# Optimization experiments

Hardware: AMD Instinct MI355X
Metric: run time of the kernel (lower is better)

## Reference

```python
import jax, jax.numpy as jnp
import numpy as np

L, S, H = 65536, 4, 256
WID = H // 2


def _linear(x, W, b):
    # eqx.nn.Linear: y = W @ x + b, W is (out, in)
    return jnp.einsum('...i,oi->...o', x, W) + b


def setup_inputs() -> dict:
    key = jax.random.key(0)
    ks = jax.random.split(key, 22)
    w = lambda k, shape: (jax.random.normal(k, shape, jnp.float32) * 0.02)
    return {
        'h': jax.random.normal(ks[0], (L, H), jnp.float32),
        'obs_stack': jax.random.normal(ks[1], (L, S, H), jnp.float32),
        'staleness_stack': jax.random.uniform(ks[2], (L, S), jnp.float32, 0.0, 10.0),
        'valid_stack': jax.random.bernoulli(ks[3], 0.8, (L, S)),
        'Wq': w(ks[4], (H, H)), 'bq': jnp.zeros((H,), jnp.float32),
        'Wk': w(ks[5], (H, H)), 'bk': jnp.zeros((H,), jnp.float32),
        'Wv': w(ks[6], (H, H)), 'bv': jnp.zeros((H,), jnp.float32),
        'null_key': jax.random.normal(ks[7], (H,), jnp.float32),
        'null_value': jax.random.normal(ks[8], (H,), jnp.float32),
        'mlp_w0': w(ks[9], (WID, 1)), 'mlp_b0': jnp.zeros((WID,), jnp.float32),
        'mlp_w1': w(ks[10], (WID, WID)), 'mlp_b1': jnp.zeros((WID,), jnp.float32),
        'mlp_w2': w(ks[11], (H, WID)), 'mlp_b2': jnp.zeros((H,), jnp.float32),
        'Wg': w(ks[12], (H, 2 * H)), 'bg': jnp.zeros((H,), jnp.float32),
        'ln_w': jnp.ones((H,), jnp.float32), 'ln_b': jnp.zeros((H,), jnp.float32),
    }


def reference(h, obs_stack, staleness_stack, valid_stack,
              Wq, bq, Wk, bk, Wv, bv, null_key, null_value,
              mlp_w0, mlp_b0, mlp_w1, mlp_b1, mlp_w2, mlp_b2,
              Wg, bg, ln_w, ln_b):
    Hd = h.shape[-1]
    Ln = h.shape[0]
    # staleness MLP (depth=2 hidden layers, relu)
    x = jnp.log1p(staleness_stack)[..., None]            # [L,S,1]
    x = jax.nn.relu(_linear(x, mlp_w0, mlp_b0))          # [L,S,W]
    x = jax.nn.relu(_linear(x, mlp_w1, mlp_b1))          # [L,S,W]
    st_emb = _linear(x, mlp_w2, mlp_b2)                  # [L,S,H]
    mod = obs_stack + st_emb
    q = _linear(h, Wq, bq)                               # [L,H]
    k = _linear(mod, Wk, bk)                             # [L,S,H]
    v = _linear(mod, Wv, bv)                             # [L,S,H]
    k = jnp.concatenate([k, jnp.broadcast_to(null_key, (Ln, 1, Hd))], axis=1)
    v = jnp.concatenate([v, jnp.broadcast_to(null_value, (Ln, 1, Hd))], axis=1)
    vmask = jnp.concatenate([valid_stack, jnp.ones((Ln, 1), bool)], axis=1)
    scores = jnp.einsum('lh,lsh->ls', q, k) / jnp.sqrt(jnp.float32(Hd))
    scores = scores + jnp.where(vmask, 0.0, -5.0)
    weights = jax.nn.softmax(scores, axis=-1)            # [L,S+1]
    fused = jnp.einsum('ls,lsh->lh', weights, v)         # [L,H]
    gate = jax.nn.sigmoid(_linear(jnp.concatenate([h, fused], axis=-1), Wg, bg))
    any_real = jnp.any(vmask[:, :-1], axis=-1, keepdims=True)
    gate = gate * any_real.astype(gate.dtype)
    mu = jnp.mean(fused, axis=-1, keepdims=True)
    var = jnp.mean((fused - mu) ** 2, axis=-1, keepdims=True)
    update = (fused - mu) / jnp.sqrt(var + 1e-5) * ln_w + ln_b
    return h + gate * update
```

## Files before the change

### kernel.cpp

```cpp
#include <hip/hip_runtime.h>
#include <math.h>


typedef __bf16 bf16x8 __attribute__((ext_vector_type(8)));
typedef float f32x4 __attribute__((ext_vector_type(4)));
typedef unsigned short u16;
typedef unsigned short u16x4 __attribute__((ext_vector_type(4)));

constexpr int Tr = 32;

constexpr int OFF_BQK = 16;
constexpr int OFF_NBK = 272;
constexpr int OFF_NQ  = 528;
constexpr int OFF_VB2P = 784;
constexpr int OFF_SCC = 1040;
constexpr size_t UOFF_QK  = 0;
constexpr size_t UOFF_X2W = 65536;
constexpr size_t UOFF_QK2 = 81920;
constexpr size_t UOFF_V   = 114688;
constexpr size_t UOFF_V2  = 180224;
constexpr size_t UOFF_G   = 212992;

constexpr int SH_QK  = 0;
constexpr int SH_QK2 = 8192;
constexpr int SH_OB  = 12288;
constexpr int SMEM_BYTES = 40960 + (384 + 128) * 4;

__device__ __forceinline__ float4 ld4(const float* p) { return *reinterpret_cast<const float4*>(p); }
__device__ __forceinline__ u16 f2bf(float x) { __bf16 b = (__bf16)x; return __builtin_bit_cast(u16, b); }
__device__ __forceinline__ float bf2f(u16 u) {
  unsigned v = ((unsigned)u) << 16;
  return __builtin_bit_cast(float, v);
}
__device__ __forceinline__ f32x4 mfma16(bf16x8 a, bf16x8 b, f32x4 c) {
  return __builtin_amdgcn_mfma_f32_16x16x32_bf16(a, b, c, 0, 0, 0);
}
__device__ __forceinline__ bf16x8 ldA8(const u16* su, int base, int stride, int row, int kcol) {
  int off = (row * stride + kcol) ^ ((row & 7) << 3);
  return *reinterpret_cast<const bf16x8*>(su + base + off);
}
__device__ __forceinline__ bf16x8 ldB8(const u16* p, size_t off) {
  return *reinterpret_cast<const bf16x8*>(p + off);
}
__device__ __forceinline__ void stBF(u16* su, int base, int stride, int row, int col, float v) {
  int off = (row * stride + col) ^ ((row & 7) << 3);
  su[base + off] = f2bf(v);
}
__device__ __forceinline__ bf16x8 ldHfrag(const float* __restrict__ h, size_t row, int k) {
  const float4 a = ld4(h + row * 256 + k);
  const float4 b = ld4(h + row * 256 + k + 4);
  bf16x8 r;
  r[0] = (__bf16)a.x; r[1] = (__bf16)a.y; r[2] = (__bf16)a.z; r[3] = (__bf16)a.w;
  r[4] = (__bf16)b.x; r[5] = (__bf16)b.y; r[6] = (__bf16)b.z; r[7] = (__bf16)b.w;
  return r;
}
__device__ __forceinline__ void barrier_lds() {
  asm volatile("s_waitcnt lgkmcnt(0)" ::: "memory");
  __builtin_amdgcn_s_barrier();
  asm volatile("" ::: "memory");
}

__global__ void k_zero(int* __restrict__ f) {
  if (threadIdx.x == 0) f[0] = 0;
}
__global__ void k_flag(const unsigned int* __restrict__ v, int nwords, int* __restrict__ flag_out) {
  int my = 0;
  for (int i = blockIdx.x * blockDim.x + threadIdx.x; i < nwords; i += gridDim.x * blockDim.x) {
    const unsigned int w = v[i];
    if (w > 1u) my |= 1;
    if (((w & 0xFFu) > 1u) || (((w >> 8) & 0xFFu) > 1u) || (((w >> 16) & 0xFFu) > 1u) ||
        ((w >> 24) > 1u))
      my |= 2;
  }
  my |= __shfl_xor(my, 32, 64);
  my |= __shfl_xor(my, 16, 64);
  my |= __shfl_xor(my, 8, 64);
  my |= __shfl_xor(my, 4, 64);
  my |= __shfl_xor(my, 2, 64);
  my |= __shfl_xor(my, 1, 64);
  if ((threadIdx.x & 63) == 0 && my) atomicOr(flag_out, my);
}

__global__ void k_prep(const float* __restrict__ Wq, const float* __restrict__ bq,
                       const float* __restrict__ Wk, const float* __restrict__ bk,
                       const float* __restrict__ Wv, const float* __restrict__ bv,
                       const float* __restrict__ nk, const float* __restrict__ w1,
                       const float* __restrict__ w2, const float* __restrict__ b2,
                       const float* __restrict__ Wg, float* __restrict__ W) {
  const int b = blockIdx.x, t = threadIdx.x;
  u16* Wu = (u16*)(W + 2048);
  __shared__ float s_tile[48 * 260];
  if (b < 672) {
    int gemm, nt, kt, KT;
    size_t ubase;
    if (b < 128)      { gemm = 0; KT = 8;  kt = b & 7;          nt = b >> 3;          ubase = UOFF_QK; }
    else if (b < 160) { gemm = 1; KT = 4;  kt = (b - 128) & 3;  nt = (b - 128) >> 2;  ubase = UOFF_X2W; }
    else if (b < 224) { gemm = 2; KT = 8;  kt = (b - 160) & 7;  nt = (b - 160) >> 3;  ubase = UOFF_QK2; }
    else if (b < 352) { gemm = 3; KT = 8;  kt = (b - 224) & 7;  nt = (b - 224) >> 3;  ubase = UOFF_V; }
    else if (b < 416) { gemm = 4; KT = 4;  kt = (b - 352) & 3;  nt = (b - 352) >> 2;  ubase = UOFF_V2; }
    else              { gemm = 5; KT = 16; kt = (b - 416) & 15; nt = (b - 416) >> 4;  ubase = UOFF_G; }
    if (gemm == 0 || gemm == 4) {
      float* sA = s_tile;
      float* sB = s_tile + 16 * 260;
      const int n0 = nt * 16, k0 = kt * 32;
      if (gemm == 0) {
        for (int idx = t; idx < 4096; idx += 256) {
          const int o = idx >> 4, n = idx & 15;
          sA[n * 260 + o] = Wk[o * 256 + n0 + n];
        }
        for (int idx = t; idx < 8192; idx += 256) {
          const int o = idx >> 5, k = idx & 31;
          sB[k * 260 + o] = Wq[o * 256 + k0 + k];
        }
      } else {
        for (int idx = t; idx < 4096; idx += 256) {
          const int n = idx >> 8, o = idx & 255;
          sA[n * 260 + o] = Wv[(size_t)(n0 + n) * 256 + o];
        }
        for (int idx = t; idx < 8192; idx += 256) {
          const int o = idx >> 5, k = idx & 31;
          sB[k * 260 + o] = w2[o * 128 + k0 + k];
        }
      }
      __syncthreads();
      for (int e = t; e < 512; e += 256) {
        const int l = e >> 3, j = e & 7;
        const int n = l & 15;
        const int k = ((l >> 4) << 3) + j;
        const float4* pa = (const float4*)(sA + n * 260);
        const float4* pb = (const float4*)(sB + k * 260);
        float acc = 0.f;
#pragma unroll 8
        for (int o4 = 0; o4 < 64; ++o4) {
          const float4 a = pa[o4], bb = pb[o4];
          acc += a.x * bb.x + a.y * bb.y + a.z * bb.z + a.w * bb.w;
        }
        Wu[ubase + (size_t)(nt * KT + kt) * 512 + e] = f2bf(acc);
      }
    } else {
      for (int e = t; e < 512; e += 256) {
        const int l = e >> 3, j = e & 7;
        const int n = nt * 16 + (l & 15);
        const int k = kt * 32 + ((l >> 4) << 3) + j;
        float val;
        if (gemm == 1)      val = w1[n * 128 + k];
        else if (gemm == 2) val = w2[k * 128 + n];
        else if (gemm == 3) val = Wv[n * 256 + k];
        else                val = Wg[n * 512 + k];
        Wu[ubase + (size_t)(nt * KT + kt) * 512 + e] = f2bf(val);
      }
    }
  } else {
    float* s_u = s_tile;
    float a = 0.f;
    for (int hh = 0; hh < 256; ++hh) a = fmaf(Wk[t * 256 + hh], b2[hh], a);
    s_u[t] = a + bk[t];
    __syncthreads();
    float a1 = 0.f, a2 = 0.f, a3 = 0.f, a4 = 0.f;
    for (int o = 0; o < 256; ++o) {
      a1 = fmaf(Wq[o * 256 + t], s_u[o], a1);
      a2 = fmaf(Wq[o * 256 + t], nk[o], a2);
      a3 = fmaf(Wk[o * 256 + t], bq[o], a3);
      a4 = fmaf(Wv[t * 256 + o], b2[o], a4);
    }
    W[OFF_NBK + t] = a1;
    W[OFF_NQ + t] = a2;
    W[OFF_BQK + t] = a3;
    W[OFF_VB2P + t] = a4 + bv[t];
    if (t == 0) {
      float c1 = 0.f, c2 = 0.f;
      for (int o = 0; o < 256; ++o) {
        c1 = fmaf(bq[o], s_u[o], c1);
        c2 = fmaf(bq[o], nk[o], c2);
      }
      W[OFF_SCC] = c1;
      W[OFF_SCC + 1] = c2;
    }
  }
}

__launch_bounds__(512) __global__
void k_main(const float* __restrict__ h, const float* __restrict__ obs,
            const float* __restrict__ stal, const void* __restrict__ valid,
            const float* __restrict__ w0, const float* __restrict__ b0,
            const float* __restrict__ b1, const float* __restrict__ bg,
            const float* __restrict__ lnw, const float* __restrict__ lnb,
            const float* __restrict__ nv, const float* __restrict__ W,
            const int* __restrict__ flagp, float* __restrict__ out) {
  extern __shared__ char smraw[];
  u16* su = (u16*)smraw;
  float* s_sc = (float*)(smraw + 40960);
  float* s_x0 = s_sc + 384;
  const u16* Wu = (const u16*)(W + 2048);
  const int t = threadIdx.x;
  const int lane = t & 63, wv = t >> 6;
  const int l16 = lane & 15, g = lane >> 4;
  const size_t row0 = (size_t)blockIdx.x * Tr;
  const int vv = *flagp;
  const int mode = ((vv & 1) == 0) ? 0 : (((vv & 2) == 0) ? 1 : 2);

  if (t < 128) {
    const int r = t >> 2, s = t & 3;
    const size_t idx = (row0 + r) * 4 + s;
    bool vb;
    if (mode == 0) vb = ((const int*)valid)[idx] != 0;
    else if (mode == 1) vb = ((const unsigned char*)valid)[idx] != 0;
    else vb = ((const float*)valid)[idx] != 0.f;
    s_sc[r * 12 + s] = vb ? 0.f : -5.f;
    s_x0[t] = log1pf(stal[idx]);
  } else if (t < 160) {
    const int r = t - 128;
    const size_t base = (row0 + r) * 4;
    bool any = false;
    for (int s = 0; s < 4; ++s) {
      bool vb;
      if (mode == 0) vb = ((const int*)valid)[base + s] != 0;
      else if (mode == 1) vb = ((const unsigned char*)valid)[base + s] != 0;
      else vb = ((const float*)valid)[base + s] != 0.f;
      any |= vb;
    }
    s_sc[r * 12 + 6] = any ? 1.f : 0.f;
  }
  barrier_lds();

  {
    const int task = lane >> 3, sub = lane & 7;
    const int r = wv * 4 + (task >> 1);
    const int which = task & 1;
    const float* vecp = which ? (W + OFF_NQ) : (W + OFF_NBK);
    const float* hp = h + (row0 + r) * 256 + sub * 32;
    const float* vp = vecp + sub * 32;
    float acc = 0.f;
#pragma unroll
    for (int j = 0; j < 8; ++j) {
      const float4 hv = ld4(hp + j * 4);
      const float4 vvv = ld4(vp + j * 4);
      acc += hv.x * vvv.x + hv.y * vvv.y + hv.z * vvv.z + hv.w * vvv.w;
    }
    acc += __shfl_xor(acc, 1, 64);
    acc += __shfl_xor(acc, 2, 64);
    acc += __shfl_xor(acc, 4, 64);
    if (sub == 0) s_sc[r * 12 + 4 + which] = acc + W[OFF_SCC + which];
  }
  {
    f32x4 acc[2][2] = {{{0.f,0.f,0.f,0.f},{0.f,0.f,0.f,0.f}},
                       {{0.f,0.f,0.f,0.f},{0.f,0.f,0.f,0.f}}};
#pragma unroll
    for (int kt = 0; kt < 8; ++kt) {
      const bf16x8 a0 = ldHfrag(h, row0 + l16, kt * 32 + g * 8);
      const bf16x8 a1 = ldHfrag(h, row0 + 16 + l16, kt * 32 + g * 8);
#pragma unroll
      for (int n2 = 0; n2 < 2; ++n2) {
        const int nt = wv * 2 + n2;
        const bf16x8 b = ldB8(Wu, UOFF_QK + (size_t)((nt * 8 + kt) * 64 + lane) * 8);
        acc[0][n2] = mfma16(a0, b, acc[0][n2]);
        acc[1][n2] = mfma16(a1, b, acc[1][n2]);
      }
    }
#pragma unroll
    for (int n2 = 0; n2 < 2; ++n2) {
      const int col = (wv * 2 + n2) * 16 + l16;
      const float bqk = W[OFF_BQK + col];
#pragma unroll
      for (int mt = 0; mt < 2; ++mt)
#pragma unroll
        for (int reg = 0; reg < 4; ++reg)
          stBF(su, SH_QK, 256, mt * 16 + g * 4 + reg, col, acc[mt][n2][reg] + bqk);
    }
  }
  bf16x8 Bq2[8];
  {
    const int ntp = (wv & 3) * 2;
#pragma unroll
    for (int i = 0; i < 8; ++i) {
      const int kt = i >> 1, n2 = i & 1;
      Bq2[i] = ldB8(Wu, UOFF_QK2 + (size_t)(((ntp + n2) * 8 + kt) * 64 + lane) * 8);
    }
  }
  barrier_lds();

  u16x4 x2p[8];
  float4 ob01[8];
  {
    const int mt = wv >> 2, ntp = (wv & 3) * 2;
    f32x4 acc2[2] = {{0.f, 0.f, 0.f, 0.f}, {0.f, 0.f, 0.f, 0.f}};
#pragma unroll
    for (int kt = 0; kt < 8; ++kt) {
      const bf16x8 a = ldA8(su, SH_QK, 256, mt * 16 + l16, kt * 32 + g * 8);
#pragma unroll
      for (int n2 = 0; n2 < 2; ++n2) {
        bf16x8 b;
        if (kt < 4) b = Bq2[kt * 2 + n2];
        else b = ldB8(Wu, UOFF_QK2 + (size_t)(((ntp + n2) * 8 + kt) * 64 + lane) * 8);
        acc2[n2] = mfma16(a, b, acc2[n2]);
      }
    }
    f32x4 accx[8] = {{0.f,0.f,0.f,0.f},{0.f,0.f,0.f,0.f},{0.f,0.f,0.f,0.f},{0.f,0.f,0.f,0.f},
                     {0.f,0.f,0.f,0.f},{0.f,0.f,0.f,0.f},{0.f,0.f,0.f,0.f},{0.f,0.f,0.f,0.f}};
    const float x0v = s_x0[wv * 16 + l16];
#pragma unroll
    for (int kt = 0; kt < 4; ++kt) {
      const int k0 = kt * 32 + g * 8;
      const float4 wa = ld4(w0 + k0), wb = ld4(w0 + k0 + 4);
      const float4 ba = ld4(b0 + k0), bb = ld4(b0 + k0 + 4);
      bf16x8 a;
      a[0] = (__bf16)fmaxf(fmaf(wa.x, x0v, ba.x), 0.f);
      a[1] = (__bf16)fmaxf(fmaf(wa.y, x0v, ba.y), 0.f);
      a[2] = (__bf16)fmaxf(fmaf(wa.z, x0v, ba.z), 0.f);
      a[3] = (__bf16)fmaxf(fmaf(wa.w, x0v, ba.w), 0.f);
      a[4] = (__bf16)fmaxf(fmaf(wb.x, x0v, bb.x), 0.f);
      a[5] = (__bf16)fmaxf(fmaf(wb.y, x0v, bb.y), 0.f);
      a[6] = (__bf16)fmaxf(fmaf(wb.z, x0v, bb.z), 0.f);
      a[7] = (__bf16)fmaxf(fmaf(wb.w, x0v, bb.w), 0.f);
#pragma unroll
      for (int nt = 0; nt < 8; ++nt) {
        const bf16x8 b = ldB8(Wu, UOFF_X2W + (size_t)((nt * 4 + kt) * 64 + lane) * 8);
        accx[nt] = mfma16(a, b, accx[nt]);
      }
    }
#pragma unroll
    for (int s = 0; s < 4; ++s) {
      ob01[s]     = ld4(obs + ((row0 + wv * 4 + 0) * 4 + s) * 256 + lane * 4);
      ob01[4 + s] = ld4(obs + ((row0 + wv * 4 + 1) * 4 + s) * 256 + lane * 4);
    }
#pragma unroll
    for (int n2 = 0; n2 < 2; ++n2) {
      const int col = (ntp + n2) * 16 + l16;
#pragma unroll
      for (int reg = 0; reg < 4; ++reg)
        su[SH_QK2 + (mt * 16 + g * 4 + reg) * 128 + col] = f2bf(acc2[n2][reg]);
    }
#pragma unroll
    for (int nt = 0; nt < 8; ++nt) {
      const int col = nt * 16 + l16;
      const float b1c = b1[col];
      u16x4 xp;
#pragma unroll
      for (int reg = 0; reg < 4; ++reg) xp[reg] = f2bf(fmaxf(accx[nt][reg] + b1c, 0.f));
      x2p[nt] = xp;
    }
  }
  barrier_lds();

  bf16x8 Vb[8];
  {
    float4 ov2[4], ov3[4];
#pragma unroll
    for (int s = 0; s < 4; ++s) {
      ov2[s] = ld4(obs + ((row0 + wv * 4 + 2) * 4 + s) * 256 + lane * 4);
      ov3[s] = ld4(obs + ((row0 + wv * 4 + 3) * 4 + s) * 256 + lane * 4);
    }
    float ep0 = 0.f, ep1 = 0.f, ep2 = 0.f, ep3 = 0.f;
    const int r_own = wv * 4 + g;
#pragma unroll
    for (int nt = 0; nt < 8; ++nt) {
      const float q2v = bf2f(su[SH_QK2 + r_own * 128 + nt * 16 + l16]);
      ep0 = fmaf(bf2f(x2p[nt][0]), q2v, ep0);
      ep1 = fmaf(bf2f(x2p[nt][1]), q2v, ep1);
      ep2 = fmaf(bf2f(x2p[nt][2]), q2v, ep2);
      ep3 = fmaf(bf2f(x2p[nt][3]), q2v, ep3);
    }
#pragma unroll
    for (int sh = 1; sh <= 8; sh <<= 1) {
      ep0 += __shfl_xor(ep0, sh, 64);
      ep1 += __shfl_xor(ep1, sh, 64);
      ep2 += __shfl_xor(ep2, sh, 64);
      ep3 += __shfl_xor(ep3, sh, 64);
    }
    float px0 = 0.f, px1 = 0.f, px2 = 0.f, px3 = 0.f;
#pragma unroll
    for (int rr = 0; rr < 4; ++rr) {
      const int r = wv * 4 + rr;
      float4 ov[4];
      if (rr == 0) { ov[0] = ob01[0]; ov[1] = ob01[1]; ov[2] = ob01[2]; ov[3] = ob01[3]; }
      else if (rr == 1) { ov[0] = ob01[4]; ov[1] = ob01[5]; ov[2] = ob01[6]; ov[3] = ob01[7]; }
      else if (rr == 2) { ov[0] = ov2[0]; ov[1] = ov2[1]; ov[2] = ov2[2]; ov[3] = ov2[3]; }
      else { ov[0] = ov3[0]; ov[1] = ov3[1]; ov[2] = ov3[2]; ov[3] = ov3[3]; }
      const int qoff = (r * 256 + lane * 4) ^ ((r & 7) << 3);
      const u16x4 qv4 = *reinterpret_cast<const u16x4*>(su + SH_QK + qoff);
      const float q0 = bf2f(qv4[0]), q1 = bf2f(qv4[1]), q2 = bf2f(qv4[2]), q3 = bf2f(qv4[3]);
      const float sbk = s_sc[r * 12 + 4];
      const float e0 = __shfl(ep0, rr << 4, 64);
      const float e1 = __shfl(ep1, rr << 4, 64);
      const float e2 = __shfl(ep2, rr << 4, 64);
      const float e3 = __shfl(ep3, rr << 4, 64);
      float sc[4];
#pragma unroll
      for (int s = 0; s < 4; ++s)
        sc[s] = q0 * ov[s].x + q1 * ov[s].y + q2 * ov[s].z + q3 * ov[s].w;
#pragma unroll
      for (int sh = 1; sh <= 32; sh <<= 1) {
#pragma unroll
        for (int s = 0; s < 4; ++s) sc[s] += __shfl_xor(sc[s], sh, 64);
      }
      sc[0] = (sc[0] + e0 + sbk) * 0.0625f + s_sc[r * 12 + 0];
      sc[1] = (sc[1] + e1 + sbk) * 0.0625f + s_sc[r * 12 + 1];
      sc[2] = (sc[2] + e2 + sbk) * 0.0625f + s_sc[r * 12 + 2];
      sc[3] = (sc[3] + e3 + sbk) * 0.0625f + s_sc[r * 12 + 3];
      const float snv = s_sc[r * 12 + 5] * 0.0625f;
      const float m = fmaxf(fmaxf(fmaxf(sc[0], sc[1]), fmaxf(sc[2], sc[3])), snv);
      const float p0e = __expf(sc[0] - m), p1e = __expf(sc[1] - m);
      const float p2e = __expf(sc[2] - m), p3e = __expf(sc[3] - m);
      const float pne = __expf(snv - m);
      const float invD = 1.f / (p0e + p1e + p2e + p3e + pne);
      const float p0 = p0e * invD, p1 = p1e * invD, p2 = p2e * invD, p3 = p3e * invD;
      const int ooff = (r * 256 + lane * 4) ^ ((r & 7) << 3);
      u16x4 o4;
      o4[0] = f2bf(p0 * ov[0].x + p1 * ov[1].x + p2 * ov[2].x + p3 * ov[3].x);
      o4[1] = f2bf(p0 * ov[0].y + p1 * ov[1].y + p2 * ov[2].y + p3 * ov[3].y);
      o4[2] = f2bf(p0 * ov[0].z + p1 * ov[1].z + p2 * ov[2].z + p3 * ov[3].z);
      o4[3] = f2bf(p0 * ov[0].w + p1 * ov[1].w + p2 * ov[2].w + p3 * ov[3].w);
      *reinterpret_cast<u16x4*>(su + SH_OB + ooff) = o4;
      if (lane == 0) s_sc[r * 12 + 7] = pne * invD;
      px0 = (rr == g) ? p0 : px0;
      px1 = (rr == g) ? p1 : px1;
      px2 = (rr == g) ? p2 : px2;
      px3 = (rr == g) ? p3 : px3;
    }
    {
      const int r = wv * 4 + g;
#pragma unroll
      for (int nt = 0; nt < 8; ++nt) {
        const int col = nt * 16 + l16;
        const float v = px0 * bf2f(x2p[nt][0]) + px1 * bf2f(x2p[nt][1]) +
                        px2 * bf2f(x2p[nt][2]) + px3 * bf2f(x2p[nt][3]);
        su[SH_QK2 + ((r * 128 + col) ^ ((r & 7) << 3))] = f2bf(v);
      }
    }
#pragma unroll
    for (int i = 0; i < 8; ++i) {
      const int kt = i >> 1, n2 = i & 1;
      Vb[i] = ldB8(Wu, UOFF_V + (size_t)(((wv * 2 + n2) * 8 + kt) * 64 + lane) * 8);
    }
  }
  barrier_lds();

  bf16x8 Gb[8];
  {
    f32x4 acc[2][2] = {{{0.f,0.f,0.f,0.f},{0.f,0.f,0.f,0.f}},
                       {{0.f,0.f,0.f,0.f},{0.f,0.f,0.f,0.f}}};
#pragma unroll
    for (int kt = 0; kt < 8; ++kt) {
      const bf16x8 a0 = ldA8(su, SH_OB, 256, l16, kt * 32 + g * 8);
      const bf16x8 a1 = ldA8(su, SH_OB, 256, 16 + l16, kt * 32 + g * 8);
#pragma unroll
      for (int n2 = 0; n2 < 2; ++n2) {
        const int nt = wv * 2 + n2;
        bf16x8 b;
        if (kt < 4) b = Vb[kt * 2 + n2];
        else b = ldB8(Wu, UOFF_V + (size_t)((nt * 8 + kt) * 64 + lane) * 8);
        acc[0][n2] = mfma16(a0, b, acc[0][n2]);
        acc[1][n2] = mfma16(a1, b, acc[1][n2]);
      }
    }
#pragma unroll
    for (int kt = 0; kt < 4; ++kt) {
      const bf16x8 a0 = ldA8(su, SH_QK2, 128, l16, kt * 32 + g * 8);
      const bf16x8 a1 = ldA8(su, SH_QK2, 128, 16 + l16, kt * 32 + g * 8);
#pragma unroll
      for (int n2 = 0; n2 < 2; ++n2) {
        const int nt = wv * 2 + n2;
        const bf16x8 b = ldB8(Wu, UOFF_V2 + (size_t)((nt * 4 + kt) * 64 + lane) * 8);
        acc[0][n2] = mfma16(a0, b, acc[0][n2]);
        acc[1][n2] = mfma16(a1, b, acc[1][n2]);
      }
    }
#pragma unroll
    for (int i = 0; i < 8; ++i) {
      const int kt = i >> 1, n2 = i & 1;
      Gb[i] = ldB8(Wu, UOFF_G + (size_t)(((wv * 2 + n2) * 16 + kt) * 64 + lane) * 8);
    }
#pragma unroll
    for (int n2 = 0; n2 < 2; ++n2) {
      const int col = (wv * 2 + n2) * 16 + l16;
      const float vb = W[OFF_VB2P + col];
      const float nvc = nv[col];
#pragma unroll
      for (int mt = 0; mt < 2; ++mt)
#pragma unroll
        for (int reg = 0; reg < 4; ++reg) {
          const int row = mt * 16 + g * 4 + reg;
          const float w4v = s_sc[row * 12 + 7];
          const float f = acc[mt][n2][reg] + (1.f - w4v) * vb + w4v * nvc;
          stBF(su, SH_QK, 256, row, col, f);
        }
    }
  }
  barrier_lds();

  {
#pragma unroll
    for (int rr = 0; rr < 4; ++rr) {
      const int r = wv * 4 + rr;
      const int foff = (r * 256 + lane * 4) ^ ((r & 7) << 3);
      const u16x4 f4 = *reinterpret_cast<const u16x4*>(su + SH_QK + foff);
      const float f0 = bf2f(f4[0]), f1 = bf2f(f4[1]), f2v = bf2f(f4[2]), f3 = bf2f(f4[3]);
      float sum = f0 + f1 + f2v + f3;
      float sq = f0 * f0 + f1 * f1 + f2v * f2v + f3 * f3;
#pragma unroll
      for (int sh = 1; sh <= 32; sh <<= 1) {
        sum += __shfl_xor(sum, sh, 64);
        sq += __shfl_xor(sq, sh, 64);
      }
      if (lane == 0) {
        const float mu = sum * (1.f / 256.f);
        const float var = sq * (1.f / 256.f) - mu * mu;
        s_sc[r * 12 + 8] = mu;
        s_sc[r * 12 + 9] = rsqrtf(var + 1e-5f);
      }
    }
  }
  {
    f32x4 acc[2][2] = {{{0.f,0.f,0.f,0.f},{0.f,0.f,0.f,0.f}},
                       {{0.f,0.f,0.f,0.f},{0.f,0.f,0.f,0.f}}};
#pragma unroll
    for (int kt = 0; kt < 8; ++kt) {
      const bf16x8 a0 = ldHfrag(h, row0 + l16, kt * 32 + g * 8);
      const bf16x8 a1 = ldHfrag(h, row0 + 16 + l16, kt * 32 + g * 8);
#pragma unroll
      for (int n2 = 0; n2 < 2; ++n2) {
        const int nt = wv * 2 + n2;
        bf16x8 b;
        if (kt < 4) b = Gb[kt * 2 + n2];
        else b = ldB8(Wu, UOFF_G + (size_t)((nt * 16 + kt) * 64 + lane) * 8);
        acc[0][n2] = mfma16(a0, b, acc[0][n2]);
        acc[1][n2] = mfma16(a1, b, acc[1][n2]);
      }
    }
#pragma unroll
    for (int kt = 8; kt < 16; ++kt) {
      const bf16x8 a0 = ldA8(su, SH_QK, 256, l16, (kt - 8) * 32 + g * 8);
      const bf16x8 a1 = ldA8(su, SH_QK, 256, 16 + l16, (kt - 8) * 32 + g * 8);
#pragma unroll
      for (int n2 = 0; n2 < 2; ++n2) {
        const int nt = wv * 2 + n2;
        const bf16x8 b = ldB8(Wu, UOFF_G + (size_t)((nt * 16 + kt) * 64 + lane) * 8);
        acc[0][n2] = mfma16(a0, b, acc[0][n2]);
        acc[1][n2] = mfma16(a1, b, acc[1][n2]);
      }
    }
#pragma unroll
    for (int n2 = 0; n2 < 2; ++n2) {
      const int col = (wv * 2 + n2) * 16 + l16;
      const float bgc = bg[col];
#pragma unroll
      for (int mt = 0; mt < 2; ++mt)
#pragma unroll
        for (int reg = 0; reg < 4; ++reg) {
          const int row = mt * 16 + g * 4 + reg;
          const float z = acc[mt][n2][reg] + bgc;
          su[SH_OB + row * 256 + col] = f2bf(1.f / (1.f + __expf(-z)));
        }
    }
  }
  barrier_lds();

  {
    const int half = t >> 8, col = t & 255;
    const float lw = lnw[col], lb = lnb[col];
#pragma unroll
    for (int i = 0; i < 16; ++i) {
      const int r = i * 2 + half;
      const float mu = s_sc[r * 12 + 8], inv = s_sc[r * 12 + 9], ar = s_sc[r * 12 + 6];
      const float f = bf2f(su[SH_QK + ((r * 256 + col) ^ ((r & 7) << 3))]);
      const float gt = bf2f(su[SH_OB + r * 256 + col]) * ar;
      const float upd = (f - mu) * inv * lw + lb;
      out[(row0 + r) * 256 + col] = h[(row0 + r) * 256 + col] + gt * upd;
    }
  }
}

extern "C" void kernel_launch(void* const* d_in, const int* in_sizes, int n_in, void* d_out,
                              int out_size, void* d_ws, size_t ws_size, hipStream_t stream) {
  const float* h = (const float*)d_in[0];
  const float* obs = (const float*)d_in[1];
  const float* st = (const float*)d_in[2];
  const void* vd = d_in[3];
  const float* Wq = (const float*)d_in[4];
  const float* bq = (const float*)d_in[5];
  const float* Wk = (const float*)d_in[6];
  const float* bk = (const float*)d_in[7];
  const float* Wv = (const float*)d_in[8];
  const float* bv = (const float*)d_in[9];
  const float* nk = (const float*)d_in[10];
  const float* nv = (const float*)d_in[11];
  const float* w0 = (const float*)d_in[12];
  const float* b0 = (const float*)d_in[13];
  const float* w1 = (const float*)d_in[14];
  const float* b1 = (const float*)d_in[15];
  const float* w2 = (const float*)d_in[16];
  const float* b2 = (const float*)d_in[17];
  const float* Wg = (const float*)d_in[18];
  const float* bg = (const float*)d_in[19];
  const float* lnw = (const float*)d_in[20];
  const float* lnb = (const float*)d_in[21];
  float* out = (float*)d_out;
  float* W = (float*)d_ws;
  const int L = in_sizes[0] / 256;

  k_zero<<<1, 64, 0, stream>>>((int*)d_ws);
  k_flag<<<256, 256, 0, stream>>>((const unsigned int*)vd, L, (int*)d_ws);
  k_prep<<<673, 256, 0, stream>>>(Wq, bq, Wk, bk, Wv, bv, nk, w1, w2, b2, Wg, W);
  k_main<<<L / Tr, 512, SMEM_BYTES, stream>>>(h, obs, st, vd, w0, b0, b1, bg, lnw, lnb, nv, W,
                                              (const int*)d_ws, out);
}
```

Before: 374.9 us.

## Halve row tile to 16 rows with 4-wave blocks and remapped MFMA tiling

Shrinks the per-block row tile from 32 to 16 and the block from 8 to 4 waves. Each wave now computes four N-tiles of a single M-tile instead of a 2x2 tile, and LDS usage is halved. The aim is more resident blocks and more blocks in the grid for better latency hiding. The cost is that each weight B-fragment is reused across only one M-tile, so weight traffic per row doubles. The diff references r_own in hidden code, so it may be partly inconsistent.

```diff
diff --git a/kernel.cpp b/kernel.cpp
--- a/kernel.cpp
+++ b/kernel.cpp
@@ -7,7 +7,7 @@
 typedef unsigned short u16;
 typedef unsigned short u16x4 __attribute__((ext_vector_type(4)));
 
-constexpr int Tr = 32;
+constexpr int Tr = 16;
 
 constexpr int OFF_BQK = 16;
 constexpr int OFF_NBK = 272;
@@ -22,9 +22,9 @@
 constexpr size_t UOFF_G   = 212992;
 
 constexpr int SH_QK  = 0;
-constexpr int SH_QK2 = 8192;
-constexpr int SH_OB  = 12288;
-constexpr int SMEM_BYTES = 40960 + (384 + 128) * 4;
+constexpr int SH_QK2 = 4096;
+constexpr int SH_OB  = 6144;
+constexpr int SMEM_BYTES = 20480 + (192 + 64) * 4;
 
 __device__ __forceinline__ float4 ld4(const float* p) { return *reinterpret_cast<const float4*>(p); }
 __device__ __forceinline__ u16 f2bf(float x) { __bf16 b = (__bf16)x; return __builtin_bit_cast(u16, b); }
@@ -35,7 +35,7 @@
 __device__ __forceinline__ f32x4 mfma16(bf16x8 a, bf16x8 b, f32x4 c) {
   return __builtin_amdgcn_mfma_f32_16x16x32_bf16(a, b, c, 0, 0, 0);
 }
-__device__ __forceinline__ bf16x8 ldA8(const u16* su, int base, int stride, int row, int kcol) {
+__device__ __forceinline__ bf16x8 ldA8g(const u16* su, int base, int stride, int row, int kcol) {
   int off = (row * stride + kcol) ^ ((row & 7) << 3);
   return *reinterpret_cast<const bf16x8*>(su + base + off);
 }
@@ -179,7 +179,7 @@
   }
 }
 
-__launch_bounds__(512) __global__
+__launch_bounds__(256) __global__
 void k_main(const float* __restrict__ h, const float* __restrict__ obs,
             const float* __restrict__ stal, const void* __restrict__ valid,
             const float* __restrict__ w0, const float* __restrict__ b0,
@@ -189,8 +189,8 @@
             const int* __restrict__ flagp, float* __restrict__ out) {
   extern __shared__ char smraw[];
   u16* su = (u16*)smraw;
-  float* s_sc = (float*)(smraw + 40960);
-  float* s_x0 = s_sc + 384;
+  float* s_sc = (float*)(smraw + 20480);
+  float* s_x0 = s_sc + 192;
   const u16* Wu = (const u16*)(W + 2048);
   const int t = threadIdx.x;
   const int lane = t & 63, wv = t >> 6;
@@ -199,7 +199,7 @@
   const int vv = *flagp;
   const int mode = ((vv & 1) == 0) ? 0 : (((vv & 2) == 0) ? 1 : 2);
 
-  if (t < 128) {
+  if (t < 64) {
     const int r = t >> 2, s = t & 3;
     const size_t idx = (row0 + r) * 4 + s;
     bool vb;
@@ -208,8 +208,8 @@
     else vb = ((const float*)valid)[idx] != 0.f;
     s_sc[r * 12 + s] = vb ? 0.f : -5.f;
     s_x0[t] = log1pf(stal[idx]);
-  } else if (t < 160) {
-    const int r = t - 128;
+  } else if (t < 80) {
+    const int r = t - 64;
     const size_t base = (row0 + r) * 4;
     bool any = false;
     for (int s = 0; s < 4; ++s) {
@@ -243,55 +243,47 @@
     if (sub == 0) s_sc[r * 12 + 4 + which] = acc + W[OFF_SCC + which];
   }
   {
-    f32x4 acc[2][2] = {{{0.f,0.f,0.f,0.f},{0.f,0.f,0.f,0.f}},
-                       {{0.f,0.f,0.f,0.f},{0.f,0.f,0.f,0.f}}};
+    f32x4 acc[4] = {{0.f, 0.f, 0.f, 0.f}, {0.f, 0.f, 0.f, 0.f},
+                    {0.f, 0.f, 0.f, 0.f}, {0.f, 0.f, 0.f, 0.f}};
 #pragma unroll
     for (int kt = 0; kt < 8; ++kt) {
       const bf16x8 a0 = ldHfrag(h, row0 + l16, kt * 32 + g * 8);
-      const bf16x8 a1 = ldHfrag(h, row0 + 16 + l16, kt * 32 + g * 8);
-#pragma unroll
-      for (int n2 = 0; n2 < 2; ++n2) {
-        const int nt = wv * 2 + n2;
+#pragma unroll
+      for (int n4 = 0; n4 < 4; ++n4) {
+        const int nt = wv * 4 + n4;
         const bf16x8 b = ldB8(Wu, UOFF_QK + (size_t)((nt * 8 + kt) * 64 + lane) * 8);
-        acc[0][n2] = mfma16(a0, b, acc[0][n2]);
-        acc[1][n2] = mfma16(a1, b, acc[1][n2]);
-      }
-    }
-#pragma unroll
-    for (int n2 = 0; n2 < 2; ++n2) {
-      const int col = (wv * 2 + n2) * 16 + l16;
+        acc[n4] = mfma16(a0, b, acc[n4]);
+      }
+    }
+#pragma unroll
+    for (int n4 = 0; n4 < 4; ++n4) {
+      const int col = (wv * 4 + n4) * 16 + l16;
       const float bqk = W[OFF_BQK + col];
 #pragma unroll
-      for (int mt = 0; mt < 2; ++mt)
-#pragma unroll
-        for (int reg = 0; reg < 4; ++reg)
-          stBF(su, SH_QK, 256, mt * 16 + g * 4 + reg, col, acc[mt][n2][reg] + bqk);
+      for (int reg = 0; reg < 4; ++reg)
+        stBF(su, SH_QK, 256, g * 4 + reg, col, acc[n4][reg] + bqk);
     }
   }
   bf16x8 Bq2[8];
-  {
-    const int ntp = (wv & 3) * 2;
-#pragma unroll
-    for (int i = 0; i < 8; ++i) {
-      const int kt = i >> 1, n2 = i & 1;
-      Bq2[i] = ldB8(Wu, UOFF_QK2 + (size_t)(((ntp + n2) * 8 + kt) * 64 + lane) * 8);
-    }
+#pragma unroll
+  for (int i = 0; i < 8; ++i) {
+    const int kt = i >> 1, n2 = i & 1;
+    Bq2[i] = ldB8(Wu, UOFF_QK2 + (size_t)(((wv * 2 + n2) * 8 + kt) * 64 + lane) * 8);
   }
   barrier_lds();
 
   u16x4 x2p[8];
   float4 ob01[8];
   {
-    const int mt = wv >> 2, ntp = (wv & 3) * 2;
     f32x4 acc2[2] = {{0.f, 0.f, 0.f, 0.f}, {0.f, 0.f, 0.f, 0.f}};
 #pragma unroll
     for (int kt = 0; kt < 8; ++kt) {
-      const bf16x8 a = ldA8(su, SH_QK, 256, mt * 16 + l16, kt * 32 + g * 8);
+      const bf16x8 a = ldA8g(su, SH_QK, 256, l16, kt * 32 + g * 8);
 #pragma unroll
       for (int n2 = 0; n2 < 2; ++n2) {
         bf16x8 b;
         if (kt < 4) b = Bq2[kt * 2 + n2];
-        else b = ldB8(Wu, UOFF_QK2 + (size_t)(((ntp + n2) * 8 + kt) * 64 + lane) * 8);
+        else b = ldB8(Wu, UOFF_QK2 + (size_t)(((wv * 2 + n2) * 8 + kt) * 64 + lane) * 8);
         acc2[n2] = mfma16(a, b, acc2[n2]);
       }
     }
@@ -325,10 +317,10 @@
     }
 #pragma unroll
     for (int n2 = 0; n2 < 2; ++n2) {
-      const int col = (ntp + n2) * 16 + l16;
+      const int col = (wv * 2 + n2) * 16 + l16;
 #pragma unroll
       for (int reg = 0; reg < 4; ++reg)
-        su[SH_QK2 + (mt * 16 + g * 4 + reg) * 128 + col] = f2bf(acc2[n2][reg]);
+        su[SH_QK2 + (g * 4 + reg) * 128 + col] = f2bf(acc2[n2][reg]);
     }
 #pragma unroll
     for (int nt = 0; nt < 8; ++nt) {
@@ -417,73 +409,64 @@
       px2 = (rr == g) ? p2 : px2;
       px3 = (rr == g) ? p3 : px3;
     }
-    {
-      const int r = wv * 4 + g;
-#pragma unroll
-      for (int nt = 0; nt < 8; ++nt) {
-        const int col = nt * 16 + l16;
-        const float v = px0 * bf2f(x2p[nt][0]) + px1 * bf2f(x2p[nt][1]) +
-                        px2 * bf2f(x2p[nt][2]) + px3 * bf2f(x2p[nt][3]);
-        su[SH_QK2 + ((r * 128 + col) ^ ((r & 7) << 3))] = f2bf(v);
-      }
+#pragma unroll
+    for (int nt = 0; nt < 8; ++nt) {
+      const int col = nt * 16 + l16;
+      const float v = px0 * bf2f(x2p[nt][0]) + px1 * bf2f(x2p[nt][1]) +
+                      px2 * bf2f(x2p[nt][2]) + px3 * bf2f(x2p[nt][3]);
+      su[SH_QK2 + ((r_own * 128 + col) ^ ((r_own & 7) << 3))] = f2bf(v);
     }
 #pragma unroll
     for (int i = 0; i < 8; ++i) {
-      const int kt = i >> 1, n2 = i & 1;
-      Vb[i] = ldB8(Wu, UOFF_V + (size_t)(((wv * 2 + n2) * 8 + kt) * 64 + lane) * 8);
+      const int kt = i >> 2, n4 = i & 3;
+      Vb[i] = ldB8(Wu, UOFF_V + (size_t)(((wv * 4 + n4) * 8 + kt) * 64 + lane) * 8);
     }
   }
   barrier_lds();
 
   bf16x8 Gb[8];
   {
-    f32x4 acc[2][2] = {{{0.f,0.f,0.f,0.f},{0.f,0.f,0.f,0.f}},
-                       {{0.f,0.f,0.f,0.f},{0.f,0.f,0.f,0.f}}};
+    f32x4 acc[4] = {{0.f, 0.f, 0.f, 0.f}, {0.f, 0.f, 0.f, 0.f},
+                    {0.f, 0.f, 0.f, 0.f}, {0.f, 0.f, 0.f, 0.f}};
 #pragma unroll
     for (int kt = 0; kt < 8; ++kt) {
-      const bf16x8 a0 = ldA8(su, SH_OB, 256, l16, kt * 32 + g * 8);
-      const bf16x8 a1 = ldA8(su, SH_OB, 256, 16 + l16, kt * 32 + g * 8);
-#pragma unroll
-      for (int n2 = 0; n2 < 2; ++n2) {
-        const int nt = wv * 2 + n2;
+      const bf16x8 a0 = ldA8g(su, SH_OB, 256, l16, kt * 32 + g * 8);
+#pragma unroll
+      for (int n4 = 0; n4 < 4; ++n4) {
+        const int nt = wv * 4 + n4;
         bf16x8 b;
-        if (kt < 4) b = Vb[kt * 2 + n2];
+        if (kt < 2) b = Vb[kt * 4 + n4];
         else b = ldB8(Wu, UOFF_V + (size_t)((nt * 8 + kt) * 64 + lane) * 8);
-        acc[0][n2] = mfma16(a0, b, acc[0][n2]);
-        acc[1][n2] = mfma16(a1, b, acc[1][n2]);
+        acc[n4] = mfma16(a0, b, acc[n4]);
       }
     }
 #pragma unroll
     for (int kt = 0; kt < 4; ++kt) {
-      const bf16x8 a0 = ldA8(su, SH_QK2, 128, l16, kt * 32 + g * 8);
-      const bf16x8 a1 = ldA8(su, SH_QK2, 128, 16 + l16, kt * 32 + g * 8);
-#pragma unroll
-      for (int n2 = 0; n2 < 2; ++n2) {
-        const int nt = wv * 2 + n2;
+      const bf16x8 a0 = ldA8g(su, SH_QK2, 128, l16, kt * 32 + g * 8);
+#pragma unroll
+      for (int n4 = 0; n4 < 4; ++n4) {
+        const int nt = wv * 4 + n4;
         const bf16x8 b = ldB8(Wu, UOFF_V2 + (size_t)((nt * 4 + kt) * 64 + lane) * 8);
-        acc[0][n2] = mfma16(a0, b, acc[0][n2]);
-        acc[1][n2] = mfma16(a1, b, acc[1][n2]);
+        acc[n4] = mfma16(a0, b, acc[n4]);
       }
     }
 #pragma unroll
     for (int i = 0; i < 8; ++i) {
-      const int kt = i >> 1, n2 = i & 1;
-      Gb[i] = ldB8(Wu, UOFF_G + (size_t)(((wv * 2 + n2) * 16 + kt) * 64 + lane) * 8);
-    }
-#pragma unroll
-    for (int n2 = 0; n2 < 2; ++n2) {
-      const int col = (wv * 2 + n2) * 16 + l16;
+      const int kt = i >> 2, n4 = i & 3;
+      Gb[i] = ldB8(Wu, UOFF_G + (size_t)(((wv * 4 + n4) * 16 + kt) * 64 + lane) * 8);
+    }
+#pragma unroll
+    for (int n4 = 0; n4 < 4; ++n4) {
+      const int col = (wv * 4 + n4) * 16 + l16;
       const float vb = W[OFF_VB2P + col];
       const float nvc = nv[col];
 #pragma unroll
-      for (int mt = 0; mt < 2; ++mt)
-#pragma unroll
-        for (int reg = 0; reg < 4; ++reg) {
-          const int row = mt * 16 + g * 4 + reg;
-          const float w4v = s_sc[row * 12 + 7];
-          const float f = acc[mt][n2][reg] + (1.f - w4v) * vb + w4v * nvc;
-          stBF(su, SH_QK, 256, row, col, f);
-        }
+      for (int reg = 0; reg < 4; ++reg) {
+        const int row = g * 4 + reg;
+        const float w4v = s_sc[row * 12 + 7];
+        const float f = acc[n4][reg] + (1.f - w4v) * vb + w4v * nvc;
+        stBF(su, SH_QK, 256, row, col, f);
+      }
     }
   }
   barrier_lds();
@@ -511,62 +494,51 @@
     }
   }
   {
-    f32x4 acc[2][2] = {{{0.f,0.f,0.f,0.f},{0.f,0.f,0.f,0.f}},
-                       {{0.f,0.f,0.f,0.f},{0.f,0.f,0.f,0.f}}};
+    f32x4 acc[4] = {{0.f, 0.f, 0.f, 0.f}, {0.f, 0.f, 0.f, 0.f},
+                    {0.f, 0.f, 0.f, 0.f}, {0.f, 0.f, 0.f, 0.f}};
 #pragma unroll
     for (int kt = 0; kt < 8; ++kt) {
       const bf16x8 a0 = ldHfrag(h, row0 + l16, kt * 32 + g * 8);
-      const bf16x8 a1 = ldHfrag(h, row0 + 16 + l16, kt * 32 + g * 8);
-#pragma unroll
-      for (int n2 = 0; n2 < 2; ++n2) {
-        const int nt = wv * 2 + n2;
+#pragma unroll
+      for (int n4 = 0; n4 < 4; ++n4) {
+        const int nt = wv * 4 + n4;
         bf16x8 b;
-        if (kt < 4) b = Gb[kt * 2 + n2];
+        if (kt < 2) b = Gb[kt * 4 + n4];
         else b = ldB8(Wu, UOFF_G + (size_t)((nt * 16 + kt) * 64 + lane) * 8);
-        acc[0][n2] = mfma16(a0, b, acc[0][n2]);
-        acc[1][n2] = mfma16(a1, b, acc[1][n2]);
+        acc[n4] = mfma16(a0, b, acc[n4]);
       }
     }
 #pragma unroll
     for (int kt = 8; kt < 16; ++kt) {
-      const bf16x8 a0 = ldA8(su, SH_QK, 256, l16, (kt - 8) * 32 + g * 8);
-      const bf16x8 a1 = ldA8(su, SH_QK, 256, 16 + l16, (kt - 8) * 32 + g * 8);
-#pragma unroll
-      for (int n2 = 0; n2 < 2; ++n2) {
-        const int nt = wv * 2 + n2;
+      const bf16x8 a0 = ldA8g(su, SH_QK, 256, l16, (kt - 8) * 32 + g * 8);
+#pragma unroll
+      for (int n4 = 0; n4 < 4; ++n4) {
+        const int nt = wv * 4 + n4;
         const bf16x8 b = ldB8(Wu, UOFF_G + (size_t)((nt * 16 + kt) * 64 + lane) * 8);
-        acc[0][n2] = mfma16(a0, b, acc[0][n2]);
-        acc[1][n2] = mfma16(a1, b, acc[1][n2]);
-      }
-    }
-#pragma unroll
-    for (int n2 = 0; n2 < 2; ++n2) {
-      const int col = (wv * 2 + n2) * 16 + l16;
+        acc[n4] = mfma16(a0, b, acc[n4]);
+      }
+    }
+#pragma unroll
+    for (int n4 = 0; n4 < 4; ++n4) {
+      const int col = (wv * 4 + n4) * 16 + l16;
       const float bgc = bg[col];
 #pragma unroll
-      for (int mt = 0; mt < 2; ++mt)
-#pragma unroll
-        for (int reg = 0; reg < 4; ++reg) {
-          const int row = mt * 16 + g * 4 + reg;
-          const float z = acc[mt][n2][reg] + bgc;
-          su[SH_OB + row * 256 + col] = f2bf(1.f / (1.f + __expf(-z)));
-        }
+      for (int reg = 0; reg < 4; ++reg) {
+        const int row = g * 4 + reg;
+        const float z = acc[n4][reg] + bgc;
+        su[SH_OB + row * 256 + col] = f2bf(1.f / (1.f + __expf(-z)));
+      }
     }
   }
   barrier_lds();
 
-  {
-    const int half = t >> 8, col = t & 255;
-    const float lw = lnw[col], lb = lnb[col];
-#pragma unroll
-    for (int i = 0; i < 16; ++i) {
-      const int r = i * 2 + half;
-      const float mu = s_sc[r * 12 + 8], inv = s_sc[r * 12 + 9], ar = s_sc[r * 12 + 6];
-      const float f = bf2f(su[SH_QK + ((r * 256 + col) ^ ((r & 7) << 3))]);
-      const float gt = bf2f(su[SH_OB + r * 256 + col]) * ar;
-      const float upd = (f - mu) * inv * lw + lb;
-      out[(row0 + r) * 256 + col] = h[(row0 + r) * 256 + col] + gt * upd;
-    }
+#pragma unroll
+  for (int i = 0; i < Tr; ++i) {
+    const float mu = s_sc[i * 12 + 8], inv = s_sc[i * 12 + 9], ar = s_sc[i * 12 + 6];
+    const float f = bf2f(su[SH_QK + ((i * 256 + t) ^ ((i & 7) << 3))]);
+    const float gt = bf2f(su[SH_OB + i * 256 + t]) * ar;
+    const float upd = (f - mu) * inv * lnw[t] + lnb[t];
+    out[(row0 + i) * 256 + t] = h[(row0 + i) * 256 + t] + gt * upd;
   }
 }
 
@@ -601,6 +573,6 @@
   k_zero<<<1, 64, 0, stream>>>((int*)d_ws);
   k_flag<<<256, 256, 0, stream>>>((const unsigned int*)vd, L, (int*)d_ws);
   k_prep<<<673, 256, 0, stream>>>(Wq, bq, Wk, bk, Wv, bv, nk, w1, w2, b2, Wg, W);
-  k_main<<<L / Tr, 512, SMEM_BYTES, stream>>>(h, obs, st, vd, w0, b0, b1, bg, lnw, lnb, nv, W,
+  k_main<<<L / Tr, 256, SMEM_BYTES, stream>>>(h, obs, st, vd, w0, b0, b1, bg, lnw, lnb, nv, W,
                                               (const int*)d_ws, out);
 }
```

Result: slower. 472.5 us (+26.0%).
